# Kernel tuning notes

Measured on AMD Instinct MI355X. Metric: run time of the kernel, lower is better.

## Reference

```python
import jax, jax.numpy as jnp
import numpy as np
from jax import lax

WIN_SIZE = 11
SIGMA = 1.5
K1, K2 = 0.01, 0.03
DATA_RANGE = 1.0


def _gaussian_window():
    coords = jnp.arange(WIN_SIZE, dtype=jnp.float32) - (WIN_SIZE - 1) / 2.0
    g = jnp.exp(-(coords ** 2) / (2.0 * SIGMA ** 2))
    return g / jnp.sum(g)


def _gaussian_filter(x, win):
    # x: (B, C, H, W); separable depthwise gaussian blur, VALID padding
    C = x.shape[1]
    dn = ('NCHW', 'OIHW', 'NCHW')
    kh = jnp.broadcast_to(win.reshape(1, 1, WIN_SIZE, 1), (C, 1, WIN_SIZE, 1))
    kw = jnp.broadcast_to(win.reshape(1, 1, 1, WIN_SIZE), (C, 1, 1, WIN_SIZE))
    x = lax.conv_general_dilated(x, kh, (1, 1), 'VALID', dimension_numbers=dn, feature_group_count=C)
    x = lax.conv_general_dilated(x, kw, (1, 1), 'VALID', dimension_numbers=dn, feature_group_count=C)
    return x


def _ssim_per_image(X, Y):
    # X, Y: (B, C, H, W) -> (B,) SSIM averaged over channels and spatial (pytorch_msssim, size_average=False)
    win = _gaussian_window()
    C1 = (K1 * DATA_RANGE) ** 2
    C2 = (K2 * DATA_RANGE) ** 2
    mu1 = _gaussian_filter(X, win)
    mu2 = _gaussian_filter(Y, win)
    mu1_sq = mu1 * mu1
    mu2_sq = mu2 * mu2
    mu1_mu2 = mu1 * mu2
    sigma1_sq = _gaussian_filter(X * X, win) - mu1_sq
    sigma2_sq = _gaussian_filter(Y * Y, win) - mu2_sq
    sigma12 = _gaussian_filter(X * Y, win) - mu1_mu2
    ssim_map = ((2.0 * mu1_mu2 + C1) * (2.0 * sigma12 + C2)) / (
        (mu1_sq + mu2_sq + C1) * (sigma1_sq + sigma2_sq + C2))
    return jnp.mean(ssim_map, axis=(1, 2, 3))


def setup_inputs() -> dict:
    key = jax.random.key(0)
    k1, k2 = jax.random.split(key)
    x1 = jax.random.normal(k1, (15, 441, 64), dtype=jnp.float32)
    x2 = jax.random.normal(k2, (5, 5, 441, 64), dtype=jnp.float32)
    return {"x1": x1, "x2": x2}


def reference(x1, x2):
    B, h, w, C = 15, 21, 21, 64
    N, S = x2.shape[0], x2.shape[1]
    # queries: view(15,21,21,64).permute(0,3,1,2) -> (15,64,21,21)
    q = jnp.transpose(x1.reshape(B, h, w, C), (0, 3, 1, 2))
    # per-(h,w) L2 normalization over channel dim (dim 0 of each sample)
    q = q / jnp.linalg.norm(q, axis=1, keepdims=True)
    # supports: (N,5,441,64).permute(0,1,3,2).view -> (N,5,64,21,21)
    s = jnp.transpose(x2, (0, 1, 3, 2)).reshape(N, S, C, h, w)
    s = s / jnp.linalg.norm(s, axis=2, keepdims=True)
    # pairwise broadcast: every query against every support image of every class
    Xb = jnp.broadcast_to(q[:, None, None], (B, N, S, C, h, w)).reshape(B * N * S, C, h, w)
    Yb = jnp.broadcast_to(s[None], (B, N, S, C, h, w)).reshape(B * N * S, C, h, w)
    sims = _ssim_per_image(Xb, Yb).reshape(B, N, S)
    # inner_sim[0, j] = sum of SSIM over the S shots
    return jnp.sum(sims, axis=2)  # (15, N)
```

## Files before the change

kernel.cpp:

```cpp
#include <hip/hip_runtime.h>

#define BQ   15
#define NIMG 40
#define CH   64
#define HW   21
#define P    441
#define WIN  11
#define OH   11
#define OP   121
#define TP   231

__device__ __forceinline__ float Wf(int a) {
    constexpr float w[WIN] = {
        0.0010283804f, 0.0075988025f, 0.0360007770f, 0.1093606993f,
        0.2130055427f, 0.2660117290f, 0.2130055427f, 0.1093606993f,
        0.0360007770f, 0.0075988025f, 0.0010283804f};
    return w[a];
}

__global__ void __launch_bounds__(256) prep_kernel(const float* __restrict__ x1,
                                                   const float* __restrict__ x2,
                                                   float* __restrict__ tn,
                                                   float* __restrict__ out) {
    if (blockIdx.x == 0 && blockIdx.y == 0 && threadIdx.x < BQ * 5)
        out[threadIdx.x] = 0.f;

    int img = blockIdx.x;
    int p0  = blockIdx.y * 63;
    const float* src = (img < BQ) ? (x1 + (size_t)img * P * CH)
                                  : (x2 + (size_t)(img - BQ) * P * CH);
    float* dst = tn + (size_t)img * CH * P;

    __shared__ float tile[63 * 65];
    __shared__ float invn[63];

    for (int i = threadIdx.x; i < 63 * CH; i += 256) {
        int p = i >> 6, c = i & 63;
        tile[p * 65 + c] = src[(size_t)p0 * CH + i];
    }
    __syncthreads();
    if (threadIdx.x < 63) {
        int p = threadIdx.x;
        float s = 0.f;
#pragma unroll
        for (int c = 0; c < CH; ++c) { float v = tile[p * 65 + c]; s += v * v; }
        invn[p] = rsqrtf(s);
    }
    __syncthreads();
    for (int i = threadIdx.x; i < 63 * CH; i += 256) {
        int c = i / 63, p = i - c * 63;
        dst[(size_t)c * P + p0 + p] = tile[p * 65 + c] * invn[p];
    }
}

__global__ void __launch_bounds__(256) stats_kernel(const float* __restrict__ tn,
                                                    float* __restrict__ mu,
                                                    float* __restrict__ sq) {
    __shared__ float lds[8 * 920];
    int cb = blockIdx.x * 8;

    for (int i = threadIdx.x; i < 8 * P; i += 256) {
        int k = i / P, t = i - k * P;
        lds[k * 920 + t] = tn[(size_t)cb * P + i];
    }
    __syncthreads();
    for (int i = threadIdx.x; i < 8 * TP; i += 256) {
        int k = i / TP, t = i - k * TP;
        const float* x = lds + k * 920;
        float a1 = 0.f, a2 = 0.f;
#pragma unroll
        for (int a = 0; a < WIN; ++a) {
            float v = x[t + 21 * a];
            a1 = fmaf(Wf(a), v, a1);
            a2 = fmaf(Wf(a) * v, v, a2);
        }
        lds[k * 920 + 448 + t] = a1;
        lds[k * 920 + 684 + t] = a2;
    }
    __syncthreads();
    for (int i = threadIdx.x; i < 8 * OP; i += 256) {
        int k = i / OP, t = i - k * OP;
        int r = t / OH, cc = t - r * OH;
        int b0 = r * HW + cc;
        const float* t1 = lds + k * 920 + 448;
        const float* t2 = lds + k * 920 + 684;
        float a1 = 0.f, a2 = 0.f;
#pragma unroll
        for (int a = 0; a < WIN; ++a) {
            a1 = fmaf(Wf(a), t1[b0 + a], a1);
            a2 = fmaf(Wf(a), t2[b0 + a], a2);
        }
        size_t o = (size_t)(cb + k) * OP + t;
        mu[o] = a1;
        sq[o] = a2;
    }
}

__global__ void __launch_bounds__(256) pairs_kernel(const float* __restrict__ tn,
                                                    const float* __restrict__ mu,
                                                    const float* __restrict__ sq,
                                                    float* __restrict__ out) {
    __shared__ float lds[8 * 684];
    __shared__ float ws4[4];

    int pair = blockIdx.x;
    int b    = pair / 25;
    int rem  = pair - b * 25;
    int cb   = blockIdx.y * 8;

    const float* X = tn + ((size_t)b * CH + cb) * P;
    const float* Y = tn + ((size_t)(BQ + rem) * CH + cb) * P;

    for (int i = threadIdx.x; i < 8 * P; i += 256) {
        int k = i / P, t = i - k * P;
        lds[k * 684 + t] = X[i] * Y[i];
    }
    __syncthreads();
    for (int i = threadIdx.x; i < 8 * TP; i += 256) {
        int k = i / TP, t = i - k * TP;
        const float* x = lds + k * 684;
        float a1 = 0.f;
#pragma unroll
        for (int a = 0; a < WIN; ++a) a1 = fmaf(Wf(a), x[t + 21 * a], a1);
        lds[k * 684 + 448 + t] = a1;
    }
    __syncthreads();

    const float C1 = 1e-4f, C2 = 9e-4f;
    size_t oq = ((size_t)b * CH + cb) * OP;
    size_t os = ((size_t)(BQ + rem) * CH + cb) * OP;
    float part = 0.f;
    for (int i = threadIdx.x; i < 8 * OP; i += 256) {
        int k = i / OP, t = i - k * OP;
        int r = t / OH, cc = t - r * OH;
        const float* t1 = lds + k * 684 + 448;
        float sxy = 0.f;
#pragma unroll
        for (int a = 0; a < WIN; ++a) sxy = fmaf(Wf(a), t1[r * HW + cc + a], sxy);
        float m1 = mu[oq + i], m2 = mu[os + i];
        float v1 = sq[oq + i] - m1 * m1;
        float v2 = sq[os + i] - m2 * m2;
        float cov = sxy - m1 * m2;
        part += ((2.f * m1 * m2 + C1) * (2.f * cov + C2)) /
                ((m1 * m1 + m2 * m2 + C1) * (v1 + v2 + C2));
    }

#pragma unroll
    for (int off = 32; off > 0; off >>= 1) part += __shfl_down(part, off, 64);
    if ((threadIdx.x & 63) == 0) ws4[threadIdx.x >> 6] = part;
    __syncthreads();
    if (threadIdx.x == 0) {
        int n = rem / 5;
        atomicAdd(&out[b * 5 + n],
                  (ws4[0] + ws4[1] + ws4[2] + ws4[3]) * (1.0f / (CH * OP)));
    }
}

extern "C" void kernel_launch(void* const* d_in, const int* in_sizes, int n_in,
                              void* d_out, int out_size, void* d_ws, size_t ws_size,
                              hipStream_t stream) {
    const float* x1 = (const float*)d_in[0];
    const float* x2 = (const float*)d_in[1];
    float* out = (float*)d_out;
    float* ws  = (float*)d_ws;

    float* tn = ws;
    float* mu = tn + (size_t)NIMG * CH * P;
    float* sq = mu + (size_t)NIMG * CH * OP;

    prep_kernel<<<dim3(NIMG, 7), 256, 0, stream>>>(x1, x2, tn, out);
    stats_kernel<<<NIMG * CH / 8, 256, 0, stream>>>(tn, mu, sq);
    pairs_kernel<<<dim3(375, 8), 256, 0, stream>>>(tn, mu, sq, out);
}
```

Measured before the change: 98.76 us.

## Fuse three phases into one cooperative persistent kernel with grid syncs

Merges the prep, stats and pairs kernels into a single cooperative kernel that loops over work units and separates phases with grid-wide barriers. Work units are made finer (21-position prep chunks, 2-channel stats units, 4-channel pair units), and the pair phase loads mu/sq into registers before the LDS work. The aim is to remove launch gaps between the three kernels and to spread the small stages across more blocks. Grid syncs cost time of their own, and smaller units repeat more per-unit overhead. A three-launch fallback is kept for when cooperative launch is unavailable.

```diff
diff --git a/kernel.cpp b/kernel.cpp
--- a/kernel.cpp
+++ b/kernel.cpp
@@ -1,4 +1,7 @@
 #include <hip/hip_runtime.h>
+#include <hip/hip_cooperative_groups.h>
+
+namespace cg = cooperative_groups;
 
 #define BQ   15
 #define NIMG 40
@@ -10,6 +13,12 @@
 #define OP   121
 #define TP   231
 
+#define P1_UNITS 840
+#define P2_UNITS 1280
+#define P3_UNITS 6000
+
+#define LDSF 2720
+
 __device__ __forceinline__ float Wf(int a) {
     constexpr float w[WIN] = {
         0.0010283804f, 0.0075988025f, 0.0360007770f, 0.1093606993f,
@@ -18,142 +27,200 @@
     return w[a];
 }
 
-__global__ void __launch_bounds__(256) prep_kernel(const float* __restrict__ x1,
-                                                   const float* __restrict__ x2,
-                                                   float* __restrict__ tn,
-                                                   float* __restrict__ out) {
-    if (blockIdx.x == 0 && blockIdx.y == 0 && threadIdx.x < BQ * 5)
-        out[threadIdx.x] = 0.f;
-
-    int img = blockIdx.x;
-    int p0  = blockIdx.y * 63;
-    const float* src = (img < BQ) ? (x1 + (size_t)img * P * CH)
-                                  : (x2 + (size_t)(img - BQ) * P * CH);
-    float* dst = tn + (size_t)img * CH * P;
-
-    __shared__ float tile[63 * 65];
-    __shared__ float invn[63];
-
-    for (int i = threadIdx.x; i < 63 * CH; i += 256) {
-        int p = i >> 6, c = i & 63;
-        tile[p * 65 + c] = src[(size_t)p0 * CH + i];
-    }
-    __syncthreads();
-    if (threadIdx.x < 63) {
-        int p = threadIdx.x;
-        float s = 0.f;
-#pragma unroll
-        for (int c = 0; c < CH; ++c) { float v = tile[p * 65 + c]; s += v * v; }
-        invn[p] = rsqrtf(s);
-    }
-    __syncthreads();
-    for (int i = threadIdx.x; i < 63 * CH; i += 256) {
-        int c = i / 63, p = i - c * 63;
-        dst[(size_t)c * P + p0 + p] = tile[p * 65 + c] * invn[p];
-    }
-}
-
-__global__ void __launch_bounds__(256) stats_kernel(const float* __restrict__ tn,
-                                                    float* __restrict__ mu,
-                                                    float* __restrict__ sq) {
-    __shared__ float lds[8 * 920];
-    int cb = blockIdx.x * 8;
-
-    for (int i = threadIdx.x; i < 8 * P; i += 256) {
-        int k = i / P, t = i - k * P;
-        lds[k * 920 + t] = tn[(size_t)cb * P + i];
-    }
-    __syncthreads();
-    for (int i = threadIdx.x; i < 8 * TP; i += 256) {
-        int k = i / TP, t = i - k * TP;
-        const float* x = lds + k * 920;
-        float a1 = 0.f, a2 = 0.f;
-#pragma unroll
-        for (int a = 0; a < WIN; ++a) {
-            float v = x[t + 21 * a];
-            a1 = fmaf(Wf(a), v, a1);
-            a2 = fmaf(Wf(a) * v, v, a2);
-        }
-        lds[k * 920 + 448 + t] = a1;
-        lds[k * 920 + 684 + t] = a2;
-    }
-    __syncthreads();
-    for (int i = threadIdx.x; i < 8 * OP; i += 256) {
-        int k = i / OP, t = i - k * OP;
-        int r = t / OH, cc = t - r * OH;
-        int b0 = r * HW + cc;
-        const float* t1 = lds + k * 920 + 448;
-        const float* t2 = lds + k * 920 + 684;
-        float a1 = 0.f, a2 = 0.f;
-#pragma unroll
-        for (int a = 0; a < WIN; ++a) {
-            a1 = fmaf(Wf(a), t1[b0 + a], a1);
-            a2 = fmaf(Wf(a), t2[b0 + a], a2);
-        }
-        size_t o = (size_t)(cb + k) * OP + t;
-        mu[o] = a1;
-        sq[o] = a2;
-    }
-}
-
-__global__ void __launch_bounds__(256) pairs_kernel(const float* __restrict__ tn,
-                                                    const float* __restrict__ mu,
-                                                    const float* __restrict__ sq,
-                                                    float* __restrict__ out) {
-    __shared__ float lds[8 * 684];
+__device__ __forceinline__ void phase_prep(const float* __restrict__ x1,
+                                           const float* __restrict__ x2,
+                                           float* __restrict__ tn,
+                                           float* __restrict__ out,
+                                           float* lds, int bid, int G) {
+    const int tid = threadIdx.x;
+    if (bid == 0 && tid < BQ * 5) out[tid] = 0.f;
+    float* invn = lds + 1408;
+    for (int u = bid; u < P1_UNITS; u += G) {
+        int img = u / 21, chunk = u - img * 21;
+        int p0 = chunk * 21;
+        const float* src = (img < BQ) ? (x1 + (size_t)img * P * CH)
+                                      : (x2 + (size_t)(img - BQ) * P * CH);
+        src += (size_t)p0 * CH;
+        float* dst = tn + (size_t)img * CH * P;
+
+        for (int i = tid; i < 21 * CH; i += 256) {
+            int p = i >> 6, c = i & 63;
+            lds[p * 65 + c] = src[i];
+        }
+        __syncthreads();
+        if (tid < 84) {
+            int p = tid >> 2, q = tid & 3;
+            const float* row = lds + p * 65 + q * 16;
+            float s = 0.f;
+#pragma unroll
+            for (int c = 0; c < 16; ++c) s = fmaf(row[c], row[c], s);
+            s += __shfl_xor(s, 1, 64);
+            s += __shfl_xor(s, 2, 64);
+            if (q == 0) invn[p] = rsqrtf(s);
+        }
+        __syncthreads();
+        for (int i = tid; i < 21 * CH; i += 256) {
+            int c = i / 21, p = i - c * 21;
+            dst[(size_t)c * P + p0 + p] = lds[p * 65 + c] * invn[p];
+        }
+        __syncthreads();
+    }
+}
+
+__device__ __forceinline__ void phase_stats(const float* __restrict__ tn,
+                                            float* __restrict__ mu,
+                                            float* __restrict__ sq,
+                                            float* lds, int bid, int G) {
+    const int tid = threadIdx.x;
+    for (int u = bid; u < P2_UNITS; u += G) {
+        int img = u >> 5, cp = u & 31;
+        const float* src = tn + ((size_t)img * CH + cp * 2) * P;
+
+        for (int i = tid; i < 2 * P; i += 256) {
+            int k = i / P, t = i - k * P;
+            lds[k * 448 + t] = src[i];
+        }
+        __syncthreads();
+        for (int i = tid; i < 2 * TP; i += 256) {
+            int k = i / TP, t = i - k * TP;
+            const float* x = lds + k * 448;
+            float a1 = 0.f, a2 = 0.f;
+#pragma unroll
+            for (int a = 0; a < WIN; ++a) {
+                float v = x[t + 21 * a];
+                a1 = fmaf(Wf(a), v, a1);
+                a2 = fmaf(Wf(a) * v, v, a2);
+            }
+            lds[896 + k * 232 + t]  = a1;
+            lds[1360 + k * 232 + t] = a2;
+        }
+        __syncthreads();
+        for (int i = tid; i < 2 * OP; i += 256) {
+            int k = i / OP, t = i - k * OP;
+            int r = t / OH, cc = t - r * OH;
+            int b0 = r * HW + cc;
+            const float* t1 = lds + 896 + k * 232;
+            const float* t2 = lds + 1360 + k * 232;
+            float a1 = 0.f, a2 = 0.f;
+#pragma unroll
+            for (int a = 0; a < WIN; ++a) {
+                a1 = fmaf(Wf(a), t1[b0 + a], a1);
+                a2 = fmaf(Wf(a), t2[b0 + a], a2);
+            }
+            size_t o = ((size_t)img * CH + cp * 2) * OP + i;
+            mu[o] = a1;
+            sq[o] = a2;
+        }
+    }
+}
+
+__device__ __forceinline__ void phase_pairs(const float* __restrict__ tn,
+                                            const float* __restrict__ mu,
+                                            const float* __restrict__ sq,
+                                            float* __restrict__ out,
+                                            float* lds, float* ws4,
+                                            int bid, int G) {
+    const float C1 = 1e-4f, C2 = 9e-4f;
+    const int tid = threadIdx.x;
+    for (int u = bid; u < P3_UNITS; u += G) {
+        int chunk = u / 375, pair = u - chunk * 375;
+        int b = pair / 25, rem = pair - b * 25;
+        int ch0 = chunk * 4;
+        const float* X = tn + ((size_t)b * CH + ch0) * P;
+        const float* Y = tn + ((size_t)(BQ + rem) * CH + ch0) * P;
+        size_t oq = ((size_t)b * CH + ch0) * OP;
+        size_t os = ((size_t)(BQ + rem) * CH + ch0) * OP;
+
+        float m1r[2], m2r[2], s1r[2], s2r[2];
+#pragma unroll
+        for (int j = 0; j < 2; ++j) {
+            int i3 = tid + j * 256;
+            int ii = (i3 < 4 * OP) ? i3 : 0;
+            m1r[j] = mu[oq + ii]; m2r[j] = mu[os + ii];
+            s1r[j] = sq[oq + ii]; s2r[j] = sq[os + ii];
+        }
+
+        for (int i = tid; i < 4 * P; i += 256) {
+            int k = i / P, t = i - k * P;
+            lds[k * 448 + t] = X[i] * Y[i];
+        }
+        __syncthreads();
+        for (int i = tid; i < 4 * TP; i += 256) {
+            int k = i / TP, t = i - k * TP;
+            const float* x = lds + k * 448;
+            float a1 = 0.f;
+#pragma unroll
+            for (int a = 0; a < WIN; ++a) a1 = fmaf(Wf(a), x[t + 21 * a], a1);
+            lds[1792 + k * 232 + t] = a1;
+        }
+        __syncthreads();
+
+        float part = 0.f;
+#pragma unroll
+        for (int j = 0; j < 2; ++j) {
+            int i3 = tid + j * 256;
+            if (i3 < 4 * OP) {
+                int k = i3 / OP, t = i3 - k * OP;
+                int r = t / OH, cc = t - r * OH;
+                const float* t1 = lds + 1792 + k * 232;
+                float sxy = 0.f;
+#pragma unroll
+                for (int a = 0; a < WIN; ++a) sxy = fmaf(Wf(a), t1[r * HW + cc + a], sxy);
+                float m1 = m1r[j], m2 = m2r[j];
+                float v1 = s1r[j] - m1 * m1;
+                float v2 = s2r[j] - m2 * m2;
+                float cov = sxy - m1 * m2;
+                part += ((2.f * m1 * m2 + C1) * (2.f * cov + C2)) /
+                        ((m1 * m1 + m2 * m2 + C1) * (v1 + v2 + C2));
+            }
+        }
+#pragma unroll
+        for (int off = 32; off > 0; off >>= 1) part += __shfl_down(part, off, 64);
+        if ((tid & 63) == 0) ws4[tid >> 6] = part;
+        __syncthreads();
+        if (tid == 0) {
+            int n = rem / 5;
+            atomicAdd(&out[b * 5 + n],
+                      (ws4[0] + ws4[1] + ws4[2] + ws4[3]) * (1.0f / (CH * OP)));
+        }
+    }
+}
+
+__global__ void __launch_bounds__(256, 5)
+fused_kernel(const float* __restrict__ x1, const float* __restrict__ x2,
+             float* __restrict__ tn, float* __restrict__ mu,
+             float* __restrict__ sq, float* __restrict__ out) {
+    __shared__ float lds[LDSF];
     __shared__ float ws4[4];
-
-    int pair = blockIdx.x;
-    int b    = pair / 25;
-    int rem  = pair - b * 25;
-    int cb   = blockIdx.y * 8;
-
-    const float* X = tn + ((size_t)b * CH + cb) * P;
-    const float* Y = tn + ((size_t)(BQ + rem) * CH + cb) * P;
-
-    for (int i = threadIdx.x; i < 8 * P; i += 256) {
-        int k = i / P, t = i - k * P;
-        lds[k * 684 + t] = X[i] * Y[i];
-    }
-    __syncthreads();
-    for (int i = threadIdx.x; i < 8 * TP; i += 256) {
-        int k = i / TP, t = i - k * TP;
-        const float* x = lds + k * 684;
-        float a1 = 0.f;
-#pragma unroll
-        for (int a = 0; a < WIN; ++a) a1 = fmaf(Wf(a), x[t + 21 * a], a1);
-        lds[k * 684 + 448 + t] = a1;
-    }
-    __syncthreads();
-
-    const float C1 = 1e-4f, C2 = 9e-4f;
-    size_t oq = ((size_t)b * CH + cb) * OP;
-    size_t os = ((size_t)(BQ + rem) * CH + cb) * OP;
-    float part = 0.f;
-    for (int i = threadIdx.x; i < 8 * OP; i += 256) {
-        int k = i / OP, t = i - k * OP;
-        int r = t / OH, cc = t - r * OH;
-        const float* t1 = lds + k * 684 + 448;
-        float sxy = 0.f;
-#pragma unroll
-        for (int a = 0; a < WIN; ++a) sxy = fmaf(Wf(a), t1[r * HW + cc + a], sxy);
-        float m1 = mu[oq + i], m2 = mu[os + i];
-        float v1 = sq[oq + i] - m1 * m1;
-        float v2 = sq[os + i] - m2 * m2;
-        float cov = sxy - m1 * m2;
-        part += ((2.f * m1 * m2 + C1) * (2.f * cov + C2)) /
-                ((m1 * m1 + m2 * m2 + C1) * (v1 + v2 + C2));
-    }
-
-#pragma unroll
-    for (int off = 32; off > 0; off >>= 1) part += __shfl_down(part, off, 64);
-    if ((threadIdx.x & 63) == 0) ws4[threadIdx.x >> 6] = part;
-    __syncthreads();
-    if (threadIdx.x == 0) {
-        int n = rem / 5;
-        atomicAdd(&out[b * 5 + n],
-                  (ws4[0] + ws4[1] + ws4[2] + ws4[3]) * (1.0f / (CH * OP)));
-    }
+    cg::grid_group g = cg::this_grid();
+    const int bid = blockIdx.x, G = gridDim.x;
+    phase_prep(x1, x2, tn, out, lds, bid, G);
+    g.sync();
+    phase_stats(tn, mu, sq, lds, bid, G);
+    g.sync();
+    phase_pairs(tn, mu, sq, out, lds, ws4, bid, G);
+}
+
+__global__ void __launch_bounds__(256) k_prep(const float* __restrict__ x1,
+                                              const float* __restrict__ x2,
+                                              float* __restrict__ tn,
+                                              float* __restrict__ out) {
+    __shared__ float lds[LDSF];
+    phase_prep(x1, x2, tn, out, lds, blockIdx.x, gridDim.x);
+}
+__global__ void __launch_bounds__(256) k_stats(const float* __restrict__ tn,
+                                               float* __restrict__ mu,
+                                               float* __restrict__ sq) {
+    __shared__ float lds[LDSF];
+    phase_stats(tn, mu, sq, lds, blockIdx.x, gridDim.x);
+}
+__global__ void __launch_bounds__(256) k_pairs(const float* __restrict__ tn,
+                                               const float* __restrict__ mu,
+                                               const float* __restrict__ sq,
+                                               float* __restrict__ out) {
+    __shared__ float lds[LDSF];
+    __shared__ float ws4[4];
+    phase_pairs(tn, mu, sq, out, lds, ws4, blockIdx.x, gridDim.x);
 }
 
 extern "C" void kernel_launch(void* const* d_in, const int* in_sizes, int n_in,
@@ -168,7 +235,30 @@
     float* mu = tn + (size_t)NIMG * CH * P;
     float* sq = mu + (size_t)NIMG * CH * OP;
 
-    prep_kernel<<<dim3(NIMG, 7), 256, 0, stream>>>(x1, x2, tn, out);
-    stats_kernel<<<NIMG * CH / 8, 256, 0, stream>>>(tn, mu, sq);
-    pairs_kernel<<<dim3(375, 8), 256, 0, stream>>>(tn, mu, sq, out);
-}
+    static int coopG = 0;
+    if (coopG == 0) {
+        int dev = 0, coop = 0, occ = 0;
+        hipGetDevice(&dev);
+        hipDeviceGetAttribute(&coop, hipDeviceAttributeCooperativeLaunch, dev);
+        hipError_t e = hipOccupancyMaxActiveBlocksPerMultiprocessor(
+            &occ, (const void*)fused_kernel, 256, 0);
+        if (coop && e == hipSuccess && occ > 0) {
+            int g = occ * 256;
+            coopG = (g > 2048) ? 2048 : g;
+        } else {
+            coopG = -1;
+        }
+    }
+    if (coopG > 0) {
+        void* args[] = {(void*)&x1, (void*)&x2, (void*)&tn,
+                        (void*)&mu, (void*)&sq, (void*)&out};
+        hipError_t e = hipLaunchCooperativeKernel((const void*)fused_kernel,
+                                                  dim3(coopG), dim3(256),
+                                                  args, 0, stream);
+        if (e == hipSuccess) return;
+        coopG = -1;
+    }
+    k_prep <<<P1_UNITS, 256, 0, stream>>>(x1, x2, tn, out);
+    k_stats<<<P2_UNITS, 256, 0, stream>>>(tn, mu, sq);
+    k_pairs<<<P3_UNITS, 256, 0, stream>>>(tn, mu, sq, out);
+}
```

Measured after the change: 336.7 us. 241% more time.
